# Kernel optimization log

Measured on AMD Instinct MI355X. Metric: run time of the kernel, lower is better.

Reference implementation:

```python
import jax, jax.numpy as jnp
import numpy as np

H = 8          # attention heads
EPS = 1e-5     # LayerNorm eps (torch default)
B, T, E = 8, 1024, 128
D, DI, N, DC, R = 512, 1024, 16, 4, 32   # d_model, d_inner, d_state, d_conv, dt_rank
NT, NM = 6, 8                            # transformer layers, mamba layers
FF = 2048                                # transformer dim_feedforward (torch default)


def setup_inputs():
    key = jax.random.key(0)
    ks = iter(jax.random.split(key, 48))
    def rn(shape, scale=0.05):
        return jax.random.normal(next(ks), shape, jnp.float32) * scale
    return {
        "emb":      jax.random.normal(next(ks), (B, T, E), jnp.float32),
        # TransformerEncoder (6 post-norm layers), params stacked on leading layer dim
        "t_wqkv":   rn((NT, 3 * E, E)), "t_bqkv": jnp.zeros((NT, 3 * E), jnp.float32),
        "t_wo":     rn((NT, E, E)),     "t_bo":   jnp.zeros((NT, E), jnp.float32),
        "t_ln1w":   jnp.ones((NT, E), jnp.float32),  "t_ln1b": jnp.zeros((NT, E), jnp.float32),
        "t_w1":     rn((NT, FF, E)),    "t_b1":   jnp.zeros((NT, FF), jnp.float32),
        "t_w2":     rn((NT, E, FF)),    "t_b2":   jnp.zeros((NT, E), jnp.float32),
        "t_ln2w":   jnp.ones((NT, E), jnp.float32),  "t_ln2b": jnp.zeros((NT, E), jnp.float32),
        # Linear(emb_dim -> d_model)
        "w_in":     rn((D, E)), "b_in": jnp.zeros((D,), jnp.float32),
        # MambaBlocks (8 raw Mamba layers, no residual/norm), stacked
        "m_inproj": rn((NM, 2 * DI, D)),
        "m_convw":  rn((NM, DI, DC), 0.2), "m_convb": jnp.zeros((NM, DI), jnp.float32),
        "m_xproj":  rn((NM, R + 2 * N, DI)),
        "m_dtw":    rn((NM, DI, R), 0.1),
        "m_dtb":    jax.random.uniform(next(ks), (NM, DI), jnp.float32, -6.0, -3.0),
        "m_Alog":   jnp.log(jnp.tile(jnp.arange(1, N + 1, dtype=jnp.float32), (NM, DI, 1))),
        "m_D":      jnp.ones((NM, DI), jnp.float32),
        "m_outproj": rn((NM, D, DI)),
        # Linear(d_model -> emb_dim)
        "w_out":    rn((E, D)), "b_out": jnp.zeros((E,), jnp.float32),
    }


def _ln(x, w, b):
    mu = jnp.mean(x, -1, keepdims=True)
    var = jnp.var(x, -1, keepdims=True)
    return (x - mu) * jax.lax.rsqrt(var + EPS) * w + b


def _tlayer(x, p):
    wqkv, bqkv, wo, bo, ln1w, ln1b, w1, b1, w2, b2, ln2w, ln2b = p
    qkv = x @ wqkv.T + bqkv                        # (B,T,3E)
    q, k, v = jnp.split(qkv, 3, axis=-1)
    def heads(t):                                  # (B,T,E) -> (B,H,T,E//H)
        return t.reshape(B, T, H, E // H).transpose(0, 2, 1, 3)
    q, k, v = heads(q), heads(k), heads(v)
    scores = jnp.einsum("bhqd,bhkd->bhqk", q, k) / jnp.sqrt(jnp.float32(E // H))
    attn = jax.nn.softmax(scores, axis=-1)
    o = jnp.einsum("bhqk,bhkd->bhqd", attn, v).transpose(0, 2, 1, 3).reshape(B, T, E)
    x = _ln(x + o @ wo.T + bo, ln1w, ln1b)         # post-norm (torch default)
    ff = jax.nn.relu(x @ w1.T + b1) @ w2.T + b2
    return _ln(x + ff, ln2w, ln2b)


def _mamba_layer(x, p):
    inproj, convw, convb, xproj, dtw, dtb, Alog, Dp, outproj = p
    xz = x @ inproj.T                              # (B,T,2*DI)
    xi, z = jnp.split(xz, 2, axis=-1)
    # causal depthwise conv1d, kernel DC, left-padded
    xp = jnp.pad(xi, ((0, 0), (DC - 1, 0), (0, 0)))
    conv = sum(xp[:, k:k + T, :] * convw[:, k] for k in range(DC)) + convb
    xi = jax.nn.silu(conv)
    dbc = xi @ xproj.T                             # (B,T,R+2N)
    dt_r, Bt, Ct = dbc[..., :R], dbc[..., R:R + N], dbc[..., R + N:]
    dt = jax.nn.softplus(dt_r @ dtw.T + dtb)       # (B,T,DI)
    A = -jnp.exp(Alog)                             # (DI,N)
    def step(h, inputs):
        dt_t, B_t, C_t, x_t = inputs               # (B,DI),(B,N),(B,N),(B,DI)
        dA = jnp.exp(dt_t[:, :, None] * A)         # (B,DI,N)
        h = h * dA + (dt_t * x_t)[:, :, None] * B_t[:, None, :]
        y = jnp.einsum("bdn,bn->bd", h, C_t)
        return h, y
    h0 = jnp.zeros((B, DI, N), x.dtype)
    seq = (dt.transpose(1, 0, 2), Bt.transpose(1, 0, 2),
           Ct.transpose(1, 0, 2), xi.transpose(1, 0, 2))
    _, ys = jax.lax.scan(step, h0, seq)            # ys: (T,B,DI)
    y = ys.transpose(1, 0, 2) + Dp * xi
    y = y * jax.nn.silu(z)
    return y @ outproj.T                           # (B,T,D)


def reference(emb, t_wqkv, t_bqkv, t_wo, t_bo, t_ln1w, t_ln1b, t_w1, t_b1, t_w2, t_b2,
              t_ln2w, t_ln2b, w_in, b_in, m_inproj, m_convw, m_convb, m_xproj, m_dtw,
              m_dtb, m_Alog, m_D, m_outproj, w_out, b_out):
    x = emb
    tparams = (t_wqkv, t_bqkv, t_wo, t_bo, t_ln1w, t_ln1b, t_w1, t_b1, t_w2, t_b2, t_ln2w, t_ln2b)
    for i in range(NT):
        x = _tlayer(x, tuple(p[i] for p in tparams))
    x = x @ w_in.T + b_in                          # (B,T,D)
    mparams = (m_inproj, m_convw, m_convb, m_xproj, m_dtw, m_dtb, m_Alog, m_D, m_outproj)
    for i in range(NM):
        x = _mamba_layer(x, tuple(p[i] for p in mparams))
    return x @ w_out.T + b_out                     # (B,T,E)
```

## Files before the change

### kernel.cpp

```cpp
#include <hip/hip_runtime.h>
#include <math.h>

#define HB 8
#define TT 1024
#define NSTATE 16
#define NTT 6
#define NMM 8
#define MM (HB*TT)
#define EPSV 1e-5f
#define CHUNK 64
#define NCH (TT/CHUNK)
#define AKS 128
#define VSTR 132

typedef _Float16 f16x8 __attribute__((ext_vector_type(8)));
typedef _Float16 f16x4 __attribute__((ext_vector_type(4)));
typedef float f32x4_t __attribute__((ext_vector_type(4)));

static __device__ __forceinline__ void split8(const float4 a, const float4 b,
                                              f16x8& h, f16x8& l)
{
  float x[8] = {a.x, a.y, a.z, a.w, b.x, b.y, b.z, b.w};
#pragma unroll
  for (int i = 0; i < 8; i++) {
    _Float16 hi = (_Float16)x[i];
    h[i] = hi;
    l[i] = (_Float16)(x[i] - (float)hi);
  }
}

static __device__ __forceinline__ void gload16(const _Float16* g, _Float16* l)
{
  __builtin_amdgcn_global_load_lds(
      (const __attribute__((address_space(1))) unsigned int*)g,
      (__attribute__((address_space(3))) unsigned int*)l, 16, 0, 0);
}

static __device__ __forceinline__ void store_split(_Float16* __restrict__ dst,
                                                   size_t row, int col, float v)
{
  const int cc = col & 31;
  const size_t o = ((size_t)(col >> 5) * MM + row) * 64
                 + (size_t)(((((cc >> 3) ^ ((int)row & 7)) * 8)) + (cc & 7));
  _Float16 hi = (_Float16)v;
  dst[o] = hi;
  dst[o ^ (size_t)32] = (_Float16)(v - (float)hi);
}

static __device__ __forceinline__ void split_item(
    const float* __restrict__ src, int lda, int rows,
    _Float16* __restrict__ dst, int item)
{
  const int m = item % rows;
  const int seg = item / rows;
  const float* s = src + (size_t)m * lda + seg * 32;
  _Float16* d = dst + (size_t)item * 64;
  const int swz = m & 7;
#pragma unroll
  for (int g = 0; g < 4; g++) {
    float4 x0 = *(const float4*)&s[g * 8];
    float4 x1 = *(const float4*)&s[g * 8 + 4];
    f16x8 h, l;
    split8(x0, x1, h, l);
    const int u = (g ^ swz) * 8;
    *(f16x8*)&d[u] = h;
    *(f16x8*)&d[u ^ 32] = l;
  }
}

__global__ __launch_bounds__(256) void split_k(
    const float* __restrict__ src, int lda, int rows,
    _Float16* __restrict__ dst)
{
  split_item(src, lda, rows, dst, blockIdx.x * 256 + threadIdx.x);
}

__global__ __launch_bounds__(256) void split3_k(
    const float* __restrict__ s0, int lda0, int rows0, _Float16* __restrict__ d0, int nb0,
    const float* __restrict__ s1, int lda1, int rows1, _Float16* __restrict__ d1, int nb1,
    const float* __restrict__ s2, int lda2, int rows2, _Float16* __restrict__ d2)
{
  const int bid = blockIdx.x;
  if (bid < nb0) {
    split_item(s0, lda0, rows0, d0, bid * 256 + threadIdx.x);
  } else if (bid < nb0 + nb1) {
    split_item(s1, lda1, rows1, d1, (bid - nb0) * 256 + threadIdx.x);
  } else {
    split_item(s2, lda2, rows2, d2, (bid - nb0 - nb1) * 256 + threadIdx.x);
  }
}

template<int TN>
__global__ __launch_bounds__(256, 4) void gemm_ps_t(
    const _Float16* __restrict__ Ap, int astr,
    const _Float16* __restrict__ Wp, int wstr,
    const float* __restrict__ bias,
    float* __restrict__ C,
    float* __restrict__ P,
    _Float16* __restrict__ Cs,
    int N, int K, int S, int act)
{
  __shared__ __align__(16) _Float16 As[128 * 64];
  __shared__ __align__(16) _Float16 Bs[TN * 64];
  const int tid = threadIdx.x;
  const int lane = tid & 63;
  const int w = tid >> 6;
  const int quad = lane >> 4;
  const int l16 = lane & 15;
  const int m0 = blockIdx.y * 128;
  const int n0 = blockIdx.x * TN;
  const int z = blockIdx.z;
  const int nseg = K / 32;
  const int segb = z * (nseg / S);
  const int sege = segb + nseg / S;

  constexpr int MI = (TN == 128) ? 4 : 2;
  const int w0 = (TN == 128) ? (w & 1) : w;
  const int w1 = (TN == 128) ? (w >> 1) : 0;
  const int rowbase = (TN == 128) ? w0 * 64 : w0 * 32;

  f32x4_t acc[MI][4];
#pragma unroll
  for (int i = 0; i < MI; i++)
#pragma unroll
    for (int j = 0; j < 4; j++)
#pragma unroll
      for (int r = 0; r < 4; r++) acc[i][j][r] = 0.f;

  const int sw8 = (quad ^ (l16 & 7)) * 8;
  const int abase = (rowbase + l16) * 64 + sw8;
  const int bbase = (w1 * 64 + l16) * 64 + sw8;
  const int wave64 = tid & 192;

  for (int seg = segb; seg < sege; seg++) {
    const _Float16* At = Ap + ((size_t)seg * astr + m0) * 64;
    const _Float16* Bt = Wp + ((size_t)seg * wstr + n0) * 64;
    __syncthreads();
#pragma unroll
    for (int j = 0; j < 4; j++)
      gload16(At + (size_t)(j * 256 + tid) * 8, &As[(j * 256 + wave64) * 8]);
#pragma unroll
    for (int j = 0; j < TN / 32; j++)
      gload16(Bt + (size_t)(j * 256 + tid) * 8, &Bs[(j * 256 + wave64) * 8]);
    __syncthreads();

    f16x8 bh[4], bl[4];
#pragma unroll
    for (int ni = 0; ni < 4; ni++) {
      bh[ni] = *(const f16x8*)&Bs[bbase + ni * 1024];
      bl[ni] = *(const f16x8*)&Bs[(bbase ^ 32) + ni * 1024];
    }
#pragma unroll
    for (int mi = 0; mi < MI; mi++) {
      f16x8 ah = *(const f16x8*)&As[abase + mi * 1024];
      f16x8 al = *(const f16x8*)&As[(abase ^ 32) + mi * 1024];
#pragma unroll
      for (int ni = 0; ni < 4; ni++) {
        acc[mi][ni] = __builtin_amdgcn_mfma_f32_16x16x32_f16(ah, bh[ni], acc[mi][ni], 0, 0, 0);
        acc[mi][ni] = __builtin_amdgcn_mfma_f32_16x16x32_f16(ah, bl[ni], acc[mi][ni], 0, 0, 0);
        acc[mi][ni] = __builtin_amdgcn_mfma_f32_16x16x32_f16(al, bh[ni], acc[mi][ni], 0, 0, 0);
      }
    }
  }

  float* dst = (S == 1) ? C : (P + (size_t)z * MM * N);
#pragma unroll
  for (int ni = 0; ni < 4; ni++) {
    const int n = n0 + w1 * 64 + ni * 16 + l16;
    const float bv = (S == 1 && bias) ? bias[n] : 0.f;
#pragma unroll
    for (int mi = 0; mi < MI; mi++) {
      const int mbase = m0 + rowbase + mi * 16 + quad * 4;
#pragma unroll
      for (int r = 0; r < 4; r++) {
        float v = acc[mi][ni][r] + bv;
        if (S == 1) {
          if (act == 1) v = fmaxf(v, 0.f);
          else if (act == 2) v = fmaxf(v, 0.f) + log1pf(__expf(-fabsf(v)));
        }
        const int row = mbase + r;
        if (S == 1 && Cs) {
          store_split(Cs, (size_t)row, n, v);
        } else {
          dst[(size_t)row * N + n] = v;
        }
      }
    }
  }
}

__global__ __launch_bounds__(256) void reduce_k(
    const float* __restrict__ P, const float* __restrict__ bias,
    float* __restrict__ C, _Float16* __restrict__ Cs,
    _Float16* __restrict__ dta,
    int nmask, int nshift, int S, int act, int stride4)
{
  const int idx = blockIdx.x * 256 + threadIdx.x;
  float4 a = *(const float4*)&P[(size_t)idx * 4];
  for (int z = 1; z < S; z++) {
    float4 p = *(const float4*)&P[(size_t)(idx + (size_t)z * stride4) * 4];
    a.x += p.x; a.y += p.y; a.z += p.z; a.w += p.w;
  }
  if (bias) {
    float4 bv = *(const float4*)&bias[(idx * 4) & nmask];
    a.x += bv.x; a.y += bv.y; a.z += bv.z; a.w += bv.w;
  }
  if (act == 1) {
    a.x = fmaxf(a.x, 0.f); a.y = fmaxf(a.y, 0.f);
    a.z = fmaxf(a.z, 0.f); a.w = fmaxf(a.w, 0.f);
  } else if (act == 2) {
    a.x = fmaxf(a.x, 0.f) + log1pf(__expf(-fabsf(a.x)));
    a.y = fmaxf(a.y, 0.f) + log1pf(__expf(-fabsf(a.y)));
    a.z = fmaxf(a.z, 0.f) + log1pf(__expf(-fabsf(a.z)));
    a.w = fmaxf(a.w, 0.f) + log1pf(__expf(-fabsf(a.w)));
  }
  const int c0 = (idx * 4) & nmask;
  const size_t row = (size_t)(idx * 4) >> nshift;
  if (Cs) {
    store_split(Cs, row, c0,     a.x);
    store_split(Cs, row, c0 + 1, a.y);
    store_split(Cs, row, c0 + 2, a.z);
    store_split(Cs, row, c0 + 3, a.w);
  } else {
    *(float4*)&C[(size_t)idx * 4] = a;
  }
  if (dta && c0 < 32) {
    store_split(dta, row, c0,     a.x);
    store_split(dta, row, c0 + 1, a.y);
    store_split(dta, row, c0 + 2, a.z);
    store_split(dta, row, c0 + 3, a.w);
  }
}

__global__ __launch_bounds__(256) void attn_mfma_k(
    const float* __restrict__ qkv, _Float16* __restrict__ os)
{
  __shared__ _Float16 Khi[AKS * 16], Klo[AKS * 16];
  __shared__ _Float16 Vthi[16 * VSTR], Vtlo[16 * VSTR];
  __shared__ float Pscr[4][16 * 18];

  const int tid = threadIdx.x;
  const int lane = tid & 63;
  const int wv = tid >> 6;
  const int quad = lane >> 4;
  const int l16 = lane & 15;
  const int qh = quad & 1;
  const int bh = blockIdx.y;
  const int b = bh >> 3;
  const int h = bh & 7;
  const int qb0 = blockIdx.x * 128;

  f16x8 qa[2];
#pragma unroll
  for (int u = 0; u < 2; u++) {
    const int qrow = qb0 + wv * 32 + u * 16 + l16;
    const float* qp = qkv + (size_t)(b * TT + qrow) * 384 + h * 16 + qh * 8;
    float4 x0 = *(const float4*)&qp[0];
    float4 x1 = *(const float4*)&qp[4];
    float xv[8] = {x0.x, x0.y, x0.z, x0.w, x1.x, x1.y, x1.z, x1.w};
#pragma unroll
    for (int j = 0; j < 8; j++) {
      float q = xv[j] * 0.25f;
      _Float16 hi = (_Float16)q;
      _Float16 lo = (_Float16)(q - (float)hi);
      qa[u][j] = (quad < 2) ? hi : lo;
    }
  }

  f32x4_t oacc[2];
  float lacc[2][4];
#pragma unroll
  for (int u = 0; u < 2; u++)
#pragma unroll
    for (int r = 0; r < 4; r++) { oacc[u][r] = 0.f; lacc[u][r] = 0.f; }

  float* Pw = &Pscr[wv][0];

  for (int ks = 0; ks < TT; ks += AKS) {
    __syncthreads();
    {
      const int key = tid >> 1, hf = tid & 1;
      const float* kp = qkv + (size_t)(b * TT + ks + key) * 384 + 128 + h * 16 + hf * 8;
      float4 k0 = *(const float4*)&kp[0];
      float4 k1 = *(const float4*)&kp[4];
      f16x8 vh, vl;
      split8(k0, k1, vh, vl);
      *(f16x8*)&Khi[key * 16 + hf * 8] = vh;
      *(f16x8*)&Klo[key * 16 + hf * 8] = vl;
      const float* vp = kp + 128;
      float4 v0 = *(const float4*)&vp[0];
      float4 v1 = *(const float4*)&vp[4];
      float vvv[8] = {v0.x, v0.y, v0.z, v0.w, v1.x, v1.y, v1.z, v1.w};
#pragma unroll
      for (int j = 0; j < 8; j++) {
        const int d = hf * 8 + j;
        _Float16 hi = (_Float16)vvv[j];
        Vthi[d * VSTR + key] = hi;
        Vtlo[d * VSTR + key] = (_Float16)(vvv[j] - (float)hi);
      }
    }
    __syncthreads();

    for (int kt = 0; kt < AKS; kt += 16) {
      f16x8 kfh = *(const f16x8*)&Khi[(kt + l16) * 16 + qh * 8];
      f16x8 kfl = *(const f16x8*)&Klo[(kt + l16) * 16 + qh * 8];
      const int vo = l16 * VSTR + kt + qh * 8;
      f16x4 va0 = *(const f16x4*)&Vthi[vo];
      f16x4 va1 = *(const f16x4*)&Vthi[vo + 4];
      f16x4 vb0 = *(const f16x4*)&Vtlo[vo];
      f16x4 vb1 = *(const f16x4*)&Vtlo[vo + 4];
      f16x8 vfh, vfl;
#pragma unroll
      for (int i = 0; i < 4; i++) {
        vfh[i] = va0[i]; vfh[4 + i] = va1[i];
        vfl[i] = vb0[i]; vfl[4 + i] = vb1[i];
      }

#pragma unroll
      for (int u = 0; u < 2; u++) {
        f32x4_t s;
#pragma unroll
        for (int r = 0; r < 4; r++) s[r] = 0.f;
        s = __builtin_amdgcn_mfma_f32_16x16x32_f16(qa[u], kfh, s, 0, 0, 0);
        s = __builtin_amdgcn_mfma_f32_16x16x32_f16(qa[u], kfl, s, 0, 0, 0);
        float p[4];
#pragma unroll
        for (int r = 0; r < 4; r++) {
          p[r] = __expf(s[r]);
          lacc[u][r] += p[r];
        }
        float* ps = Pw + (quad * 4) * 18 + l16;
        ps[0] = p[0]; ps[18] = p[1]; ps[36] = p[2]; ps[54] = p[3];
        __asm__ volatile("s_waitcnt lgkmcnt(0)" ::: "memory");
        const float* pr = Pw + l16 * 18 + qh * 8;
        f16x8 pa;
#pragma unroll
        for (int j = 0; j < 8; j++) {
          float pv = pr[j];
          _Float16 hi = (_Float16)pv;
          _Float16 lo = (_Float16)(pv - (float)hi);
          pa[j] = (quad < 2) ? hi : lo;
        }
        oacc[u] = __builtin_amdgcn_mfma_f32_16x16x32_f16(pa, vfh, oacc[u], 0, 0, 0);
        oacc[u] = __builtin_amdgcn_mfma_f32_16x16x32_f16(pa, vfl, oacc[u], 0, 0, 0);
        __asm__ volatile("s_waitcnt lgkmcnt(0)" ::: "memory");
      }
    }
  }

#pragma unroll
  for (int u = 0; u < 2; u++) {
#pragma unroll
    for (int r = 0; r < 4; r++) {
      float lv = lacc[u][r];
      lv += __shfl_xor(lv, 1);
      lv += __shfl_xor(lv, 2);
      lv += __shfl_xor(lv, 4);
      lv += __shfl_xor(lv, 8);
      const float inv = 1.f / lv;
      const int qrow = qb0 + wv * 32 + u * 16 + quad * 4 + r;
      const size_t m = (size_t)(b * TT + qrow);
      store_split(os, m, h * 16 + l16, oacc[u][r] * inv);
    }
  }
}

__global__ __launch_bounds__(256) void add_ln_k(
    const float* __restrict__ a, const float* __restrict__ bvec,
    const float* __restrict__ w, const float* __restrict__ bb,
    float* __restrict__ out, _Float16* __restrict__ outs)
{
  const int tid = threadIdx.x;
  const int wave = tid >> 6, lane = tid & 63;
  const size_t row = (size_t)blockIdx.x * 4 + wave;
  const float* pa = a + row * 128;
  const float* pb = bvec + row * 128;
  float v0 = pa[lane] + pb[lane];
  float v1 = pa[lane + 64] + pb[lane + 64];
  float s1 = v0 + v1, s2 = v0 * v0 + v1 * v1;
#pragma unroll
  for (int off = 32; off; off >>= 1) {
    s1 += __shfl_down(s1, off);
    s2 += __shfl_down(s2, off);
  }
  s1 = __shfl(s1, 0); s2 = __shfl(s2, 0);
  const float mean = s1 * (1.f / 128.f);
  const float var = s2 * (1.f / 128.f) - mean * mean;
  const float rs = rsqrtf(var + EPSV);
  const float o0 = (v0 - mean) * rs * w[lane] + bb[lane];
  const float o1 = (v1 - mean) * rs * w[lane + 64] + bb[lane + 64];
  out[row * 128 + lane] = o0;
  out[row * 128 + lane + 64] = o1;
  store_split(outs, row, lane, o0);
  store_split(outs, row, lane + 64, o1);
}

__global__ __launch_bounds__(256) void conv_silu_k(
    const float* __restrict__ xz, const float* __restrict__ cw,
    const float* __restrict__ cb, float* __restrict__ out,
    _Float16* __restrict__ outs)
{
  const int idx = blockIdx.x * 256 + threadIdx.x;
  const int di = idx & 1023;
  const int m = idx >> 10;
  const int t = m & (TT - 1);
  float acc = cb[di];
#pragma unroll
  for (int k = 0; k < 4; k++) {
    int tt = t + k - 3;
    if (tt >= 0) acc += xz[(size_t)(m + k - 3) * 2048 + di] * cw[di * 4 + k];
  }
  const float y = acc / (1.f + __expf(-acc));
  out[(size_t)m * 1024 + di] = y;
  store_split(outs, (size_t)m, di, y);
}

__global__ __launch_bounds__(64) void scan_partial_k(
    const float* __restrict__ dt,
    const float* __restrict__ dbc,
    const float* __restrict__ xi,
    const float* __restrict__ Alog,
    float* __restrict__ Pb, float* __restrict__ Sb)
{
  const int slice = blockIdx.x & 15;
  const int c = blockIdx.x >> 4;
  const int b = blockIdx.y;
  const int di = slice * 64 + threadIdx.x;

  float A[NSTATE];
#pragma unroll
  for (int n = 0; n < NSTATE; n++) A[n] = -__expf(Alog[di * NSTATE + n]);
  float h[NSTATE], P[NSTATE];
#pragma unroll
  for (int n = 0; n < NSTATE; n++) { h[n] = 0.f; P[n] = 1.f; }

  const size_t m0 = (size_t)b * TT + (size_t)c * CHUNK;
  for (int t = 0; t < CHUNK; t++) {
    const size_t m = m0 + t;
    const float dtv = dt[m * 1024 + di];
    const float xv  = xi[m * 1024 + di];
    const float dtx = dtv * xv;
#pragma unroll
    for (int n = 0; n < NSTATE; n++) {
      const float Bv = dbc[m * 64 + 32 + n];
      const float dA = __expf(dtv * A[n]);
      h[n] = h[n] * dA + dtx * Bv;
      P[n] *= dA;
    }
  }
  const size_t base = (((size_t)b * NCH + c) * NSTATE) * 1024 + di;
#pragma unroll
  for (int n = 0; n < NSTATE; n++) {
    Pb[base + (size_t)n * 1024] = P[n];
    Sb[base + (size_t)n * 1024] = h[n];
  }
}

__global__ __launch_bounds__(256) void scan_fix_k(
    float* __restrict__ Pb, const float* __restrict__ Sb)
{
  const int idx = blockIdx.x * 256 + threadIdx.x;
  const int b = idx >> 10;
  const int di = idx & 1023;
  float h[NSTATE];
#pragma unroll
  for (int n = 0; n < NSTATE; n++) h[n] = 0.f;
  for (int c = 0; c < NCH; c++) {
    const size_t base = (((size_t)b * NCH + c) * NSTATE) * 1024 + di;
    float P[NSTATE], S[NSTATE];
#pragma unroll
    for (int n = 0; n < NSTATE; n++) {
      P[n] = Pb[base + (size_t)n * 1024];
      S[n] = Sb[base + (size_t)n * 1024];
    }
#pragma unroll
    for (int n = 0; n < NSTATE; n++) {
      Pb[base + (size_t)n * 1024] = h[n];
      h[n] = P[n] * h[n] + S[n];
    }
  }
}

__global__ __launch_bounds__(64) void scan_final_k(
    const float* __restrict__ dt,
    const float* __restrict__ dbc,
    const float* __restrict__ xi,
    const float* __restrict__ xz,
    const float* __restrict__ Alog,
    const float* __restrict__ Dp,
    const float* __restrict__ Hin,
    _Float16* __restrict__ Y)
{
  const int slice = blockIdx.x & 15;
  const int c = blockIdx.x >> 4;
  const int b = blockIdx.y;
  const int di = slice * 64 + threadIdx.x;

  float A[NSTATE];
#pragma unroll
  for (int n = 0; n < NSTATE; n++) A[n] = -__expf(Alog[di * NSTATE + n]);
  const float Dv = Dp[di];
  float h[NSTATE];
  const size_t hbase = (((size_t)b * NCH + c) * NSTATE) * 1024 + di;
#pragma unroll
  for (int n = 0; n < NSTATE; n++) h[n] = Hin[hbase + (size_t)n * 1024];

  const size_t m0 = (size_t)b * TT + (size_t)c * CHUNK;
  for (int t = 0; t < CHUNK; t++) {
    const size_t m = m0 + t;
    const float dtv = dt[m * 1024 + di];
    const float xv  = xi[m * 1024 + di];
    const float zv  = xz[m * 2048 + 1024 + di];
    const float dtx = dtv * xv;
    float y = 0.f;
#pragma unroll
    for (int n = 0; n < NSTATE; n++) {
      const float Bv = dbc[m * 64 + 32 + n];
      const float Cv = dbc[m * 64 + 48 + n];
      const float dA = __expf(dtv * A[n]);
      h[n] = h[n] * dA + dtx * Bv;
      y += h[n] * Cv;
    }
    y += Dv * xv;
    y *= zv / (1.f + __expf(-zv));
    store_split(Y, m, di, y);
  }
}

extern "C" void kernel_launch(void* const* d_in, const int* in_sizes, int n_in,
                              void* d_out, int out_size, void* d_ws, size_t ws_size,
                              hipStream_t stream)
{
  (void)in_sizes; (void)n_in; (void)out_size; (void)ws_size;
  const float* emb      = (const float*)d_in[0];
  const float* t_wqkv   = (const float*)d_in[1];
  const float* t_bqkv   = (const float*)d_in[2];
  const float* t_wo     = (const float*)d_in[3];
  const float* t_bo     = (const float*)d_in[4];
  const float* t_ln1w   = (const float*)d_in[5];
  const float* t_ln1b   = (const float*)d_in[6];
  const float* t_w1     = (const float*)d_in[7];
  const float* t_b1     = (const float*)d_in[8];
  const float* t_w2     = (const float*)d_in[9];
  const float* t_b2     = (const float*)d_in[10];
  const float* t_ln2w   = (const float*)d_in[11];
  const float* t_ln2b   = (const float*)d_in[12];
  const float* w_in     = (const float*)d_in[13];
  const float* b_in     = (const float*)d_in[14];
  const float* m_inproj = (const float*)d_in[15];
  const float* m_convw  = (const float*)d_in[16];
  const float* m_convb  = (const float*)d_in[17];
  const float* m_xproj  = (const float*)d_in[18];
  const float* m_dtw    = (const float*)d_in[19];
  const float* m_dtb    = (const float*)d_in[20];
  const float* m_Alog   = (const float*)d_in[21];
  const float* m_D      = (const float*)d_in[22];
  const float* m_outproj= (const float*)d_in[23];
  const float* w_out    = (const float*)d_in[24];
  const float* b_out    = (const float*)d_in[25];

  float* ws = (float*)d_ws;
  float* R1 = ws;
  float* R2 = ws + (size_t)MM * 512;
  float* R3 = ws + (size_t)MM * 1024;
  float* R4 = ws + (size_t)MM * 3072;
  float* R5 = ws + (size_t)MM * 4096;
  float* R6 = ws + (size_t)MM * 5120;
  float* R7 = ws + (size_t)MM * 6144;

  _Float16* TWQKV = (_Float16*)R4;
  _Float16* TWO   = TWQKV + (size_t)294912 * 2;
  _Float16* TW1   = TWO   + (size_t)98304 * 2;
  _Float16* TW2   = TW1   + (size_t)1572864 * 2;
  _Float16* TWIN  = TW2   + (size_t)1572864 * 2;

  _Float16* ASP1 = (_Float16*)R6;
  _Float16* XIS  = (_Float16*)R6;
  _Float16* DTA  = (_Float16*)R6;
  _Float16* YSP  = (_Float16*)R6;

  dim3 blk(256);
  auto split = [&](const float* src, int lda, int rows, int K, _Float16* dst) {
    hipLaunchKernelGGL(split_k, dim3(rows * (K / 32) / 256), blk, 0, stream,
                       src, lda, rows, dst);
  };
  auto gemm = [&](const _Float16* Ap, const _Float16* Wp, int wstr,
                  const float* bias, float* C, int N, int K, int act,
                  int S, float* P, _Float16* Cs, _Float16* dta, bool tn64) {
    dim3 g(N / (tn64 ? 64 : 128), MM / 128, S);
    if (tn64)
      hipLaunchKernelGGL(gemm_ps_t<64>, g, blk, 0, stream,
                         Ap, MM, Wp, wstr, bias, C, P, Cs, N, K, S, act);
    else
      hipLaunchKernelGGL(gemm_ps_t<128>, g, blk, 0, stream,
                         Ap, MM, Wp, wstr, bias, C, P, Cs, N, K, S, act);
    if (S > 1) {
      int stride4 = (int)((size_t)MM * N / 4);
      hipLaunchKernelGGL(reduce_k, dim3(stride4 / 256), blk, 0, stream,
                         P, bias, C, Cs, dta, N - 1, __builtin_ctz(N), S, act,
                         stride4);
    }
  };

  split(t_wqkv, 128,  2304,  128, TWQKV);
  split(t_wo,   128,   768,  128, TWO);
  split(t_w1,   128, 12288,  128, TW1);
  split(t_w2,  2048,   768, 2048, TW2);
  split(w_in,   128,   512,  128, TWIN);
  split(emb,    128,    MM,  128, ASP1);

  const float* x = emb;
  for (int l = 0; l < NTT; l++) {
    gemm(ASP1, TWQKV + (size_t)l * 384 * 64, 2304, t_bqkv + l * 384,
         R3, 384, 128, 0, 1, nullptr, nullptr, nullptr, false);
    hipLaunchKernelGGL(attn_mfma_k, dim3(TT / 128, HB * 8), blk, 0, stream,
                       R3, ASP1);
    gemm(ASP1, TWO + (size_t)l * 128 * 64, 768, t_bo + l * 128,
         R5, 128, 128, 0, 2, R2, nullptr, nullptr, true);
    hipLaunchKernelGGL(add_ln_k, dim3(MM / 4), blk, 0, stream,
                       x, R5, t_ln1w + l * 128, t_ln1b + l * 128, R1, ASP1);
    gemm(ASP1, TW1 + (size_t)l * 2048 * 64, 12288, t_b1 + l * 2048,
         R3, 2048, 128, 1, 1, nullptr, (_Float16*)R3, nullptr, false);
    gemm((_Float16*)R3, TW2 + (size_t)l * 128 * 64, 768, t_b2 + l * 128,
         R5, 128, 2048, 0, 8, R6, nullptr, nullptr, false);
    hipLaunchKernelGGL(add_ln_k, dim3(MM / 4), blk, 0, stream,
                       R1, R5, t_ln2w + l * 128, t_ln2b + l * 128, R1, ASP1);
    x = R1;
  }

  gemm(ASP1, TWIN, 512, b_in, R2, 512, 128, 0, 1, nullptr, (_Float16*)R2,
       nullptr, false);

  float* xcs = R2;
  float* xos = R1;
  for (int l = 0; l < NMM; l++) {
    _Float16* WIs = (_Float16*)(xos + (size_t)MM * 256);
    _Float16* WXs = (_Float16*)(xos + (size_t)MM * 384);
    _Float16* WDs = (_Float16*)(xos + (size_t)MM * 392);
    _Float16* WOs = (_Float16*)(xos + (size_t)MM * 256);
    hipLaunchKernelGGL(split3_k, dim3(140), blk, 0, stream,
        m_inproj + (size_t)l * 2048 * 512, 512, 2048, WIs, 128,
        m_xproj  + (size_t)l * 64 * 1024, 1024,   64, WXs,   8,
        m_dtw    + (size_t)l * 1024 * 32,   32, 1024, WDs);

    gemm((_Float16*)xcs, WIs, 2048, nullptr,
         R3, 2048, 512, 0, 1, nullptr, nullptr, nullptr, false);
    hipLaunchKernelGGL(conv_silu_k, dim3(MM * 1024 / 256), blk, 0, stream,
                       R3, m_convw + (size_t)l * 1024 * 4, m_convb + l * 1024,
                       R4, XIS);
    gemm(XIS, WXs, 64, nullptr,
         R7, 64, 1024, 0, 4, xos, nullptr, DTA, true);
    gemm(DTA, WDs, 1024, m_dtb + l * 1024,
         R5, 1024, 32, 2, 1, nullptr, nullptr, nullptr, false);

    float* Pb = xos;
    float* Sb = xos + (size_t)MM * 256;
    hipLaunchKernelGGL(scan_partial_k, dim3(16 * NCH, HB), dim3(64), 0, stream,
                       R5, R7, R4, m_Alog + (size_t)l * 1024 * 16, Pb, Sb);
    hipLaunchKernelGGL(scan_fix_k, dim3(MM / 1024 * 4), blk, 0, stream, Pb, Sb);
    split(m_outproj + (size_t)l * 512 * 1024, 1024, 512, 1024, WOs);
    hipLaunchKernelGGL(scan_final_k, dim3(16 * NCH, HB), dim3(64), 0, stream,
                       R5, R7, R4, R3,
                       m_Alog + (size_t)l * 1024 * 16, m_D + l * 1024, Pb, YSP);

    gemm(YSP, WOs, 512, nullptr,
         R5, 512, 1024, 0, 2, R3, (_Float16*)xos, nullptr, false);
    float* ts = xcs; xcs = xos; xos = ts;
  }

  _Float16* WOUTs = (_Float16*)xos;
  split(w_out, 512, 128, 512, WOUTs);
  gemm((_Float16*)xcs, WOUTs, 128, b_out,
       (float*)d_out, 128, 512, 0, 4, R6, nullptr, nullptr, false);
}
```

Baseline: 3.779 ms.

## Emit pre-split K/V from QKV GEMM, restructure attention, vectorize elementwise kernels

The QKV GEMM epilogue now writes K and V directly as swizzled hi/lo fp16 layouts. The attention kernel can then load them into LDS with async global_load_lds instead of reconverting fp32 on every tile, and it uses 64-query blocks with one 16-row tile per wave. The six initial weight/input split launches are merged into one kernel. conv_silu, scan_final and the reduce epilogue now process two channels per thread with paired fp16 stores. Together these aim to cut redundant conversion work, launch count and narrow memory accesses, at the cost of extra scratch buffers and halving the scan_final grid.

```diff
diff --git a/kernel.cpp b/kernel.cpp
--- a/kernel.cpp
+++ b/kernel.cpp
@@ -11,10 +11,10 @@
 #define CHUNK 64
 #define NCH (TT/CHUNK)
 #define AKS 128
-#define VSTR 132
 
 typedef _Float16 f16x8 __attribute__((ext_vector_type(8)));
 typedef _Float16 f16x4 __attribute__((ext_vector_type(4)));
+typedef _Float16 f16x2 __attribute__((ext_vector_type(2)));
 typedef float f32x4_t __attribute__((ext_vector_type(4)));
 
 static __device__ __forceinline__ void split8(const float4 a, const float4 b,
@@ -45,6 +45,20 @@
   _Float16 hi = (_Float16)v;
   dst[o] = hi;
   dst[o ^ (size_t)32] = (_Float16)(v - (float)hi);
+}
+
+static __device__ __forceinline__ void store_split2(_Float16* __restrict__ dst,
+                                                    size_t row, int col0,
+                                                    float v0, float v1)
+{
+  const int cc = col0 & 31;
+  const size_t o = ((size_t)(col0 >> 5) * MM + row) * 64
+                 + (size_t)(((((cc >> 3) ^ ((int)row & 7)) * 8)) + (cc & 7));
+  _Float16 h0 = (_Float16)v0, h1 = (_Float16)v1;
+  f16x2 hp = {h0, h1};
+  f16x2 lp = {(_Float16)(v0 - (float)h0), (_Float16)(v1 - (float)h1)};
+  *(f16x2*)&dst[o] = hp;
+  *(f16x2*)&dst[o ^ (size_t)32] = lp;
 }
 
 static __device__ __forceinline__ void split_item(
@@ -90,6 +104,23 @@
   }
 }
 
+__global__ __launch_bounds__(256) void split6_k(
+    const float* __restrict__ s0, int lda0, int rows0, _Float16* __restrict__ d0, int c0,
+    const float* __restrict__ s1, int lda1, int rows1, _Float16* __restrict__ d1, int c1,
+    const float* __restrict__ s2, int lda2, int rows2, _Float16* __restrict__ d2, int c2,
+    const float* __restrict__ s3, int lda3, int rows3, _Float16* __restrict__ d3, int c3,
+    const float* __restrict__ s4, int lda4, int rows4, _Float16* __restrict__ d4, int c4,
+    const float* __restrict__ s5, int lda5, int rows5, _Float16* __restrict__ d5)
+{
+  const int bid = blockIdx.x;
+  if (bid < c0)      split_item(s0, lda0, rows0, d0, bid * 256 + threadIdx.x);
+  else if (bid < c1) split_item(s1, lda1, rows1, d1, (bid - c0) * 256 + threadIdx.x);
+  else if (bid < c2) split_item(s2, lda2, rows2, d2, (bid - c1) * 256 + threadIdx.x);
+  else if (bid < c3) split_item(s3, lda3, rows3, d3, (bid - c2) * 256 + threadIdx.x);
+  else if (bid < c4) split_item(s4, lda4, rows4, d4, (bid - c3) * 256 + threadIdx.x);
+  else               split_item(s5, lda5, rows5, d5, (bid - c4) * 256 + threadIdx.x);
+}
+
 template<int TN>
 __global__ __launch_bounds__(256, 4) void gemm_ps_t(
     const _Float16* __restrict__ Ap, int astr,
@@ -98,6 +129,8 @@
     float* __restrict__ C,
     float* __restrict__ P,
     _Float16* __restrict__ Cs,
+    _Float16* __restrict__ Ks,
+    _Float16* __restrict__ Vs,
     int N, int K, int S, int act)
 {
   __shared__ __align__(16) _Float16 As[128 * 64];
@@ -163,6 +196,41 @@
     }
   }
 
+  if (Ks && n0 >= 128) {
+    const bool isK = (n0 == 128);
+#pragma unroll
+    for (int ni = 0; ni < 4; ni++) {
+      const int n = n0 + w1 * 64 + ni * 16 + l16;
+      const float bv = bias ? bias[n] : 0.f;
+      const int hh = w1 * 4 + ni;
+#pragma unroll
+      for (int mi = 0; mi < MI; mi++) {
+        const int mbase = m0 + rowbase + mi * 16 + quad * 4;
+#pragma unroll
+        for (int r = 0; r < 4; r++) {
+          const float v = acc[mi][ni][r] + bv;
+          const int row = mbase + r;
+          const int key = row & (TT - 1);
+          const int bh8 = (row >> 10) * 8 + hh;
+          _Float16 hi = (_Float16)v;
+          _Float16 lo = (_Float16)(v - (float)hi);
+          if (isK) {
+            const int p = ((l16 >> 3) + (key >> 1)) & 3;
+            const size_t kb = (((size_t)bh8 << 10) + key) * 32 + (l16 & 7);
+            Ks[kb + p * 8] = hi;
+            Ks[kb + (p ^ 2) * 8] = lo;
+          } else {
+            const int k2 = (key & ~127) | ((key & 127) ^ (l16 * 8));
+            const size_t vb = ((size_t)bh8 * 32 + l16) * 1024 + k2;
+            Vs[vb] = hi;
+            Vs[vb + 16 * 1024] = lo;
+          }
+        }
+      }
+    }
+    return;
+  }
+
   float* dst = (S == 1) ? C : (P + (size_t)z * MM * N);
 #pragma unroll
   for (int ni = 0; ni < 4; ni++) {
@@ -217,26 +285,25 @@
   const int c0 = (idx * 4) & nmask;
   const size_t row = (size_t)(idx * 4) >> nshift;
   if (Cs) {
-    store_split(Cs, row, c0,     a.x);
-    store_split(Cs, row, c0 + 1, a.y);
-    store_split(Cs, row, c0 + 2, a.z);
-    store_split(Cs, row, c0 + 3, a.w);
+    store_split2(Cs, row, c0,     a.x, a.y);
+    store_split2(Cs, row, c0 + 2, a.z, a.w);
   } else {
     *(float4*)&C[(size_t)idx * 4] = a;
   }
   if (dta && c0 < 32) {
-    store_split(dta, row, c0,     a.x);
-    store_split(dta, row, c0 + 1, a.y);
-    store_split(dta, row, c0 + 2, a.z);
-    store_split(dta, row, c0 + 3, a.w);
+    store_split2(dta, row, c0,     a.x, a.y);
+    store_split2(dta, row, c0 + 2, a.z, a.w);
   }
 }
 
 __global__ __launch_bounds__(256) void attn_mfma_k(
-    const float* __restrict__ qkv, _Float16* __restrict__ os)
-{
-  __shared__ _Float16 Khi[AKS * 16], Klo[AKS * 16];
-  __shared__ _Float16 Vthi[16 * VSTR], Vtlo[16 * VSTR];
+    const float* __restrict__ qkv,
+    const _Float16* __restrict__ Kg,
+    const _Float16* __restrict__ Vg,
+    _Float16* __restrict__ os)
+{
+  __shared__ __align__(16) _Float16 Klds[AKS * 32];
+  __shared__ __align__(16) _Float16 Vlds[32 * AKS];
   __shared__ float Pscr[4][16 * 18];
 
   const int tid = threadIdx.x;
@@ -248,12 +315,12 @@
   const int bh = blockIdx.y;
   const int b = bh >> 3;
   const int h = bh & 7;
-  const int qb0 = blockIdx.x * 128;
-
-  f16x8 qa[2];
-#pragma unroll
-  for (int u = 0; u < 2; u++) {
-    const int qrow = qb0 + wv * 32 + u * 16 + l16;
+  const int qb0 = blockIdx.x * 64;
+  const int wave64 = tid & 192;
+
+  f16x8 qa;
+  {
+    const int qrow = qb0 + wv * 16 + l16;
     const float* qp = qkv + (size_t)(b * TT + qrow) * 384 + h * 16 + qh * 8;
     float4 x0 = *(const float4*)&qp[0];
     float4 x1 = *(const float4*)&qp[4];
@@ -263,105 +330,87 @@
       float q = xv[j] * 0.25f;
       _Float16 hi = (_Float16)q;
       _Float16 lo = (_Float16)(q - (float)hi);
-      qa[u][j] = (quad < 2) ? hi : lo;
-    }
-  }
-
-  f32x4_t oacc[2];
-  float lacc[2][4];
-#pragma unroll
-  for (int u = 0; u < 2; u++)
-#pragma unroll
-    for (int r = 0; r < 4; r++) { oacc[u][r] = 0.f; lacc[u][r] = 0.f; }
+      qa[j] = (quad < 2) ? hi : lo;
+    }
+  }
+
+  f32x4_t oacc;
+  float lacc[4];
+#pragma unroll
+  for (int r = 0; r < 4; r++) { oacc[r] = 0.f; lacc[r] = 0.f; }
 
   float* Pw = &Pscr[wv][0];
+  const _Float16* Kb = Kg + (((size_t)bh) << 10) * 32;
+  const _Float16* Vb = Vg + ((size_t)bh * 32) * 1024;
 
   for (int ks = 0; ks < TT; ks += AKS) {
     __syncthreads();
     {
-      const int key = tid >> 1, hf = tid & 1;
-      const float* kp = qkv + (size_t)(b * TT + ks + key) * 384 + 128 + h * 16 + hf * 8;
-      float4 k0 = *(const float4*)&kp[0];
-      float4 k1 = *(const float4*)&kp[4];
-      f16x8 vh, vl;
-      split8(k0, k1, vh, vl);
-      *(f16x8*)&Khi[key * 16 + hf * 8] = vh;
-      *(f16x8*)&Klo[key * 16 + hf * 8] = vl;
-      const float* vp = kp + 128;
-      float4 v0 = *(const float4*)&vp[0];
-      float4 v1 = *(const float4*)&vp[4];
-      float vvv[8] = {v0.x, v0.y, v0.z, v0.w, v1.x, v1.y, v1.z, v1.w};
+      const _Float16* Kt = Kb + (size_t)ks * 32;
+#pragma unroll
+      for (int it = 0; it < 2; it++) {
+        const int cb = it * 256 + tid;
+        gload16(Kt + (size_t)cb * 8, &Klds[(it * 256 + wave64) * 8]);
+      }
+#pragma unroll
+      for (int it = 0; it < 2; it++) {
+        const int cb = it * 256 + tid;
+        const int rowv = cb >> 4, co = cb & 15;
+        gload16(Vb + (size_t)rowv * 1024 + ks + co * 8,
+                &Vlds[(it * 256 + wave64) * 8]);
+      }
+    }
+    __syncthreads();
+
+    for (int kt = 0; kt < AKS; kt += 16) {
+      const int key = kt + l16;
+      const int ph = (qh + (key >> 1)) & 3;
+      f16x8 kfh = *(const f16x8*)&Klds[key * 32 + ph * 8];
+      f16x8 kfl = *(const f16x8*)&Klds[key * 32 + (ph ^ 2) * 8];
+      const int vko = (kt + qh * 8) ^ (l16 * 8);
+      f16x8 vfh = *(const f16x8*)&Vlds[l16 * 128 + vko];
+      f16x8 vfl = *(const f16x8*)&Vlds[(16 + l16) * 128 + vko];
+
+      f32x4_t s;
+#pragma unroll
+      for (int r = 0; r < 4; r++) s[r] = 0.f;
+      s = __builtin_amdgcn_mfma_f32_16x16x32_f16(qa, kfh, s, 0, 0, 0);
+      s = __builtin_amdgcn_mfma_f32_16x16x32_f16(qa, kfl, s, 0, 0, 0);
+      float p[4];
+#pragma unroll
+      for (int r = 0; r < 4; r++) {
+        p[r] = __expf(s[r]);
+        lacc[r] += p[r];
+      }
+      float* ps = Pw + (quad * 4) * 18 + l16;
+      ps[0] = p[0]; ps[18] = p[1]; ps[36] = p[2]; ps[54] = p[3];
+      __asm__ volatile("s_waitcnt lgkmcnt(0)" ::: "memory");
+      const float* pr = Pw + l16 * 18 + qh * 8;
+      f16x8 pa;
 #pragma unroll
       for (int j = 0; j < 8; j++) {
-        const int d = hf * 8 + j;
-        _Float16 hi = (_Float16)vvv[j];
-        Vthi[d * VSTR + key] = hi;
-        Vtlo[d * VSTR + key] = (_Float16)(vvv[j] - (float)hi);
+        float pv = pr[j];
+        _Float16 hi = (_Float16)pv;
+        _Float16 lo = (_Float16)(pv - (float)hi);
+        pa[j] = (quad < 2) ? hi : lo;
       }
-    }
-    __syncthreads();
-
-    for (int kt = 0; kt < AKS; kt += 16) {
-      f16x8 kfh = *(const f16x8*)&Khi[(kt + l16) * 16 + qh * 8];
-      f16x8 kfl = *(const f16x8*)&Klo[(kt + l16) * 16 + qh * 8];
-      const int vo = l16 * VSTR + kt + qh * 8;
-      f16x4 va0 = *(const f16x4*)&Vthi[vo];
-      f16x4 va1 = *(const f16x4*)&Vthi[vo + 4];
-      f16x4 vb0 = *(const f16x4*)&Vtlo[vo];
-      f16x4 vb1 = *(const f16x4*)&Vtlo[vo + 4];
-      f16x8 vfh, vfl;
-#pragma unroll
-      for (int i = 0; i < 4; i++) {
-        vfh[i] = va0[i]; vfh[4 + i] = va1[i];
-        vfl[i] = vb0[i]; vfl[4 + i] = vb1[i];
-      }
-
-#pragma unroll
-      for (int u = 0; u < 2; u++) {
-        f32x4_t s;
-#pragma unroll
-        for (int r = 0; r < 4; r++) s[r] = 0.f;
-        s = __builtin_amdgcn_mfma_f32_16x16x32_f16(qa[u], kfh, s, 0, 0, 0);
-        s = __builtin_amdgcn_mfma_f32_16x16x32_f16(qa[u], kfl, s, 0, 0, 0);
-        float p[4];
-#pragma unroll
-        for (int r = 0; r < 4; r++) {
-          p[r] = __expf(s[r]);
-          lacc[u][r] += p[r];
-        }
-        float* ps = Pw + (quad * 4) * 18 + l16;
-        ps[0] = p[0]; ps[18] = p[1]; ps[36] = p[2]; ps[54] = p[3];
-        __asm__ volatile("s_waitcnt lgkmcnt(0)" ::: "memory");
-        const float* pr = Pw + l16 * 18 + qh * 8;
-        f16x8 pa;
-#pragma unroll
-        for (int j = 0; j < 8; j++) {
-          float pv = pr[j];
-          _Float16 hi = (_Float16)pv;
-          _Float16 lo = (_Float16)(pv - (float)hi);
-          pa[j] = (quad < 2) ? hi : lo;
-        }
-        oacc[u] = __builtin_amdgcn_mfma_f32_16x16x32_f16(pa, vfh, oacc[u], 0, 0, 0);
-        oacc[u] = __builtin_amdgcn_mfma_f32_16x16x32_f16(pa, vfl, oacc[u], 0, 0, 0);
-        __asm__ volatile("s_waitcnt lgkmcnt(0)" ::: "memory");
-      }
-    }
-  }
-
-#pragma unroll
-  for (int u = 0; u < 2; u++) {
-#pragma unroll
-    for (int r = 0; r < 4; r++) {
-      float lv = lacc[u][r];
-      lv += __shfl_xor(lv, 1);
-      lv += __shfl_xor(lv, 2);
-      lv += __shfl_xor(lv, 4);
-      lv += __shfl_xor(lv, 8);
-      const float inv = 1.f / lv;
-      const int qrow = qb0 + wv * 32 + u * 16 + quad * 4 + r;
-      const size_t m = (size_t)(b * TT + qrow);
-      store_split(os, m, h * 16 + l16, oacc[u][r] * inv);
-    }
+      oacc = __builtin_amdgcn_mfma_f32_16x16x32_f16(pa, vfh, oacc, 0, 0, 0);
+      oacc = __builtin_amdgcn_mfma_f32_16x16x32_f16(pa, vfl, oacc, 0, 0, 0);
+      __asm__ volatile("s_waitcnt lgkmcnt(0)" ::: "memory");
+    }
+  }
+
+#pragma unroll
+  for (int r = 0; r < 4; r++) {
+    float lv = lacc[r];
+    lv += __shfl_xor(lv, 1);
+    lv += __shfl_xor(lv, 2);
+    lv += __shfl_xor(lv, 4);
+    lv += __shfl_xor(lv, 8);
+    const float inv = 1.f / lv;
+    const int qrow = qb0 + wv * 16 + quad * 4 + r;
+    const size_t m = (size_t)(b * TT + qrow);
+    store_split(os, m, h * 16 + l16, oacc[r] * inv);
   }
 }
 
@@ -401,18 +450,24 @@
     _Float16* __restrict__ outs)
 {
   const int idx = blockIdx.x * 256 + threadIdx.x;
-  const int di = idx & 1023;
-  const int m = idx >> 10;
+  const int di = (idx & 511) * 2;
+  const int m = idx >> 9;
   const int t = m & (TT - 1);
-  float acc = cb[di];
+  float a0 = cb[di], a1 = cb[di + 1];
 #pragma unroll
   for (int k = 0; k < 4; k++) {
     int tt = t + k - 3;
-    if (tt >= 0) acc += xz[(size_t)(m + k - 3) * 2048 + di] * cw[di * 4 + k];
-  }
-  const float y = acc / (1.f + __expf(-acc));
-  out[(size_t)m * 1024 + di] = y;
-  store_split(outs, (size_t)m, di, y);
+    if (tt >= 0) {
+      float2 xv = *(const float2*)&xz[(size_t)(m + k - 3) * 2048 + di];
+      a0 += xv.x * cw[di * 4 + k];
+      a1 += xv.y * cw[(di + 1) * 4 + k];
+    }
+  }
+  const float y0 = a0 / (1.f + __expf(-a0));
+  const float y1 = a1 / (1.f + __expf(-a1));
+  float2 yo = {y0, y1};
+  *(float2*)&out[(size_t)m * 1024 + di] = yo;
+  store_split2(outs, (size_t)m, di, y0, y1);
 }
 
 __global__ __launch_bounds__(64) void scan_partial_k(
@@ -491,39 +546,51 @@
     const float* __restrict__ Hin,
     _Float16* __restrict__ Y)
 {
-  const int slice = blockIdx.x & 15;
-  const int c = blockIdx.x >> 4;
+  const int slice = blockIdx.x & 7;
+  const int c = blockIdx.x >> 3;
   const int b = blockIdx.y;
-  const int di = slice * 64 + threadIdx.x;
-
-  float A[NSTATE];
-#pragma unroll
-  for (int n = 0; n < NSTATE; n++) A[n] = -__expf(Alog[di * NSTATE + n]);
-  const float Dv = Dp[di];
-  float h[NSTATE];
+  const int di = slice * 128 + threadIdx.x * 2;
+
+  float A0[NSTATE], A1[NSTATE];
+#pragma unroll
+  for (int n = 0; n < NSTATE; n++) {
+    A0[n] = -__expf(Alog[di * NSTATE + n]);
+    A1[n] = -__expf(Alog[(di + 1) * NSTATE + n]);
+  }
+  const float Dv0 = Dp[di], Dv1 = Dp[di + 1];
+  float h0[NSTATE], h1[NSTATE];
   const size_t hbase = (((size_t)b * NCH + c) * NSTATE) * 1024 + di;
 #pragma unroll
-  for (int n = 0; n < NSTATE; n++) h[n] = Hin[hbase + (size_t)n * 1024];
+  for (int n = 0; n < NSTATE; n++) {
+    h0[n] = Hin[hbase + (size_t)n * 1024];
+    h1[n] = Hin[hbase + (size_t)n * 1024 + 1];
+  }
 
   const size_t m0 = (size_t)b * TT + (size_t)c * CHUNK;
   for (int t = 0; t < CHUNK; t++) {
     const size_t m = m0 + t;
-    const float dtv = dt[m * 1024 + di];
-    const float xv  = xi[m * 1024 + di];
-    const float zv  = xz[m * 2048 + 1024 + di];
-    const float dtx = dtv * xv;
-    float y = 0.f;
+    const float2 dtv = *(const float2*)&dt[m * 1024 + di];
+    const float2 xv  = *(const float2*)&xi[m * 1024 + di];
+    const float2 zv  = *(const float2*)&xz[m * 2048 + 1024 + di];
+    const float dtx0 = dtv.x * xv.x;
+    const float dtx1 = dtv.y * xv.y;
+    float y0 = 0.f, y1 = 0.f;
 #pragma unroll
     for (int n = 0; n < NSTATE; n++) {
       const float Bv = dbc[m * 64 + 32 + n];
       const float Cv = dbc[m * 64 + 48 + n];
-      const float dA = __expf(dtv * A[n]);
-      h[n] = h[n] * dA + dtx * Bv;
-      y += h[n] * Cv;
-    }
-    y += Dv * xv;
-    y *= zv / (1.f + __expf(-zv));
-    store_split(Y, m, di, y);
+      const float dA0 = __expf(dtv.x * A0[n]);
+      const float dA1 = __expf(dtv.y * A1[n]);
+      h0[n] = h0[n] * dA0 + dtx0 * Bv;
+      h1[n] = h1[n] * dA1 + dtx1 * Bv;
+      y0 += h0[n] * Cv;
+      y1 += h1[n] * Cv;
+    }
+    y0 += Dv0 * xv.x;
+    y1 += Dv1 * xv.y;
+    y0 *= zv.x / (1.f + __expf(-zv.x));
+    y1 *= zv.y / (1.f + __expf(-zv.y));
+    store_split2(Y, m, di, y0, y1);
   }
 }
 
@@ -579,6 +646,9 @@
   _Float16* DTA  = (_Float16*)R6;
   _Float16* YSP  = (_Float16*)R6;
 
+  _Float16* KG = (_Float16*)(R2 + (size_t)MM * 256);
+  _Float16* VG = (_Float16*)(R2 + (size_t)MM * 320);
+
   dim3 blk(256);
   auto split = [&](const float* src, int lda, int rows, int K, _Float16* dst) {
     hipLaunchKernelGGL(split_k, dim3(rows * (K / 32) / 256), blk, 0, stream,
@@ -586,14 +656,15 @@
   };
   auto gemm = [&](const _Float16* Ap, const _Float16* Wp, int wstr,
                   const float* bias, float* C, int N, int K, int act,
-                  int S, float* P, _Float16* Cs, _Float16* dta, bool tn64) {
+                  int S, float* P, _Float16* Cs, _Float16* dta,
+                  _Float16* Ks, _Float16* Vs, bool tn64) {
     dim3 g(N / (tn64 ? 64 : 128), MM / 128, S);
     if (tn64)
       hipLaunchKernelGGL(gemm_ps_t<64>, g, blk, 0, stream,
-                         Ap, MM, Wp, wstr, bias, C, P, Cs, N, K, S, act);
+                         Ap, MM, Wp, wstr, bias, C, P, Cs, Ks, Vs, N, K, S, act);
     else
       hipLaunchKernelGGL(gemm_ps_t<128>, g, blk, 0, stream,
-                         Ap, MM, Wp, wstr, bias, C, P, Cs, N, K, S, act);
+                         Ap, MM, Wp, wstr, bias, C, P, Cs, Ks, Vs, N, K, S, act);
     if (S > 1) {
       int stride4 = (int)((size_t)MM * N / 4);
       hipLaunchKernelGGL(reduce_k, dim3(stride4 / 256), blk, 0, stream,
@@ -602,34 +673,35 @@
     }
   };
 
-  split(t_wqkv, 128,  2304,  128, TWQKV);
-  split(t_wo,   128,   768,  128, TWO);
-  split(t_w1,   128, 12288,  128, TW1);
-  split(t_w2,  2048,   768, 2048, TW2);
-  split(w_in,   128,   512,  128, TWIN);
-  split(emb,    128,    MM,  128, ASP1);
+  hipLaunchKernelGGL(split6_k, dim3(568), blk, 0, stream,
+      t_wqkv, 128,  2304, TWQKV,  36,
+      t_wo,   128,   768, TWO,    48,
+      t_w1,   128, 12288, TW1,   240,
+      t_w2,  2048,   768, TW2,   432,
+      w_in,   128,   512, TWIN,  440,
+      emb,    128,    MM, ASP1);
 
   const float* x = emb;
   for (int l = 0; l < NTT; l++) {
     gemm(ASP1, TWQKV + (size_t)l * 384 * 64, 2304, t_bqkv + l * 384,
-         R3, 384, 128, 0, 1, nullptr, nullptr, nullptr, false);
-    hipLaunchKernelGGL(attn_mfma_k, dim3(TT / 128, HB * 8), blk, 0, stream,
-                       R3, ASP1);
+         R3, 384, 128, 0, 1, nullptr, nullptr, nullptr, KG, VG, false);
+    hipLaunchKernelGGL(attn_mfma_k, dim3(TT / 64, HB * 8), blk, 0, stream,
+                       R3, KG, VG, ASP1);
     gemm(ASP1, TWO + (size_t)l * 128 * 64, 768, t_bo + l * 128,
-         R5, 128, 128, 0, 2, R2, nullptr, nullptr, true);
+         R5, 128, 128, 0, 2, R2, nullptr, nullptr, nullptr, nullptr, true);
     hipLaunchKernelGGL(add_ln_k, dim3(MM / 4), blk, 0, stream,
                        x, R5, t_ln1w + l * 128, t_ln1b + l * 128, R1, ASP1);
     gemm(ASP1, TW1 + (size_t)l * 2048 * 64, 12288, t_b1 + l * 2048,
-         R3, 2048, 128, 1, 1, nullptr, (_Float16*)R3, nullptr, false);
+         R3, 2048, 128, 1, 1, nullptr, (_Float16*)R3, nullptr, nullptr, nullptr, false);
     gemm((_Float16*)R3, TW2 + (size_t)l * 128 * 64, 768, t_b2 + l * 128,
-         R5, 128, 2048, 0, 8, R6, nullptr, nullptr, false);
+         R5, 128, 2048, 0, 8, R6, nullptr, nullptr, nullptr, nullptr, false);
     hipLaunchKernelGGL(add_ln_k, dim3(MM / 4), blk, 0, stream,
                        R1, R5, t_ln2w + l * 128, t_ln2b + l * 128, R1, ASP1);
     x = R1;
   }
 
   gemm(ASP1, TWIN, 512, b_in, R2, 512, 128, 0, 1, nullptr, (_Float16*)R2,
-       nullptr, false);
+       nullptr, nullptr, nullptr, false);
 
   float* xcs = R2;
   float* xos = R1;
@@ -644,14 +716,14 @@
         m_dtw    + (size_t)l * 1024 * 32,   32, 1024, WDs);
 
     gemm((_Float16*)xcs, WIs, 2048, nullptr,
-         R3, 2048, 512, 0, 1, nullptr, nullptr, nullptr, false);
-    hipLaunchKernelGGL(conv_silu_k, dim3(MM * 1024 / 256), blk, 0, stream,
+         R3, 2048, 512, 0, 1, nullptr, nullptr, nullptr, nullptr, nullptr, false);
+    hipLaunchKernelGGL(conv_silu_k, dim3(MM * 512 / 256), blk, 0, stream,
                        R3, m_convw + (size_t)l * 1024 * 4, m_convb + l * 1024,
                        R4, XIS);
     gemm(XIS, WXs, 64, nullptr,
-         R7, 64, 1024, 0, 4, xos, nullptr, DTA, true);
+         R7, 64, 1024, 0, 4, xos, nullptr, DTA, nullptr, nullptr, true);
     gemm(DTA, WDs, 1024, m_dtb + l * 1024,
-         R5, 1024, 32, 2, 1, nullptr, nullptr, nullptr, false);
+         R5, 1024, 32, 2, 1, nullptr, nullptr, nullptr, nullptr, nullptr, false);
 
     float* Pb = xos;
     float* Sb = xos + (size_t)MM * 256;
@@ -659,17 +731,17 @@
                        R5, R7, R4, m_Alog + (size_t)l * 1024 * 16, Pb, Sb);
     hipLaunchKernelGGL(scan_fix_k, dim3(MM / 1024 * 4), blk, 0, stream, Pb, Sb);
     split(m_outproj + (size_t)l * 512 * 1024, 1024, 512, 1024, WOs);
-    hipLaunchKernelGGL(scan_final_k, dim3(16 * NCH, HB), dim3(64), 0, stream,
+    hipLaunchKernelGGL(scan_final_k, dim3(8 * NCH, HB), dim3(64), 0, stream,
                        R5, R7, R4, R3,
                        m_Alog + (size_t)l * 1024 * 16, m_D + l * 1024, Pb, YSP);
 
     gemm(YSP, WOs, 512, nullptr,
-         R5, 512, 1024, 0, 2, R3, (_Float16*)xos, nullptr, false);
+         R5, 512, 1024, 0, 2, R3, (_Float16*)xos, nullptr, nullptr, nullptr, false);
     float* ts = xcs; xcs = xos; xos = ts;
   }
 
   _Float16* WOUTs = (_Float16*)xos;
   split(w_out, 512, 128, 512, WOUTs);
   gemm((_Float16*)xcs, WOUTs, 128, b_out,
-       (float*)d_out, 128, 512, 0, 4, R6, nullptr, nullptr, false);
-}
+       (float*)d_out, 128, 512, 0, 4, R6, nullptr, nullptr, nullptr, nullptr, false);
+}
```

New measurement: 4.615 ms. 1.22x slower.
